# Kernel tuning notes

Hardware: AMD Instinct MI355X
Metric: run time of the kernel (lower is better)

Reference implementation:

```python
import jax, jax.numpy as jnp
import numpy as np

NDIM = 1024
NHEAD = 16
HEAD_DIM = NDIM // NHEAD


def setup_inputs() -> dict:
    key = jax.random.key(0)
    ks = jax.random.split(key, 12)
    B, L, C = 2, 2048, NDIM
    s = 0.02
    return {
        "q": jax.random.normal(ks[0], (B, L, C), jnp.float32),
        "k": jax.random.normal(ks[1], (B, L, C), jnp.float32),
        "v": jax.random.normal(ks[2], (B, L, C), jnp.float32),
        "Wq": jax.random.normal(ks[3], (C, C), jnp.float32) * s,
        "bq": jax.random.normal(ks[4], (C,), jnp.float32) * s,
        "Wk": jax.random.normal(ks[5], (C, C), jnp.float32) * s,
        "bk": jax.random.normal(ks[6], (C,), jnp.float32) * s,
        "Wv": jax.random.normal(ks[7], (C, C), jnp.float32) * s,
        "bv": jax.random.normal(ks[8], (C,), jnp.float32) * s,
        "Wo": jax.random.normal(ks[9], (C, C), jnp.float32) * s,
        "bo": jax.random.normal(ks[10], (C,), jnp.float32) * s,
    }


def reference(q, k, v, Wq, bq, Wk, bk, Wv, bv, Wo, bo):
    B, Lq, C = q.shape
    H, D = NHEAD, HEAD_DIM
    # projections, then split heads: (B, H, L, D)
    qh = (q @ Wq + bq).reshape(B, Lq, H, D).transpose(0, 2, 1, 3)
    kh = (k @ Wk + bk).reshape(B, k.shape[1], H, D).transpose(0, 2, 1, 3)
    vh = (v @ Wv + bv).reshape(B, v.shape[1], H, D).transpose(0, 2, 1, 3)
    scale = 1.0 / jnp.sqrt(jnp.asarray(D, qh.dtype))
    att = jnp.einsum("bhqd,bhkd->bhqk", qh, kh) * scale  # (B,H,Lq,Lk)
    att = jax.nn.softmax(att, axis=-1)  # dropout p=0.0 -> identity
    y = jnp.einsum("bhqk,bhkd->bhqd", att, vh)
    y = y.transpose(0, 2, 1, 3).reshape(B, Lq, C)
    return y @ Wo + bo
```

## Files before the change

### kernel.cpp

```cpp
#include <hip/hip_runtime.h>
#include <math.h>

#define BATCH 2
#define SEQ   2048
#define CDIM  1024
#define NHEAD 16
#define HDIM  64
#define TOKS  (BATCH * SEQ)

typedef __bf16 bf16x8 __attribute__((ext_vector_type(8)));
typedef __bf16 bf16x2 __attribute__((ext_vector_type(2)));
typedef float  f32x4  __attribute__((ext_vector_type(4)));

#define MFMA16(a, b, c) __builtin_amdgcn_mfma_f32_16x16x32_bf16(a, b, c, 0, 0, 0)

#define QSCALE 0.1803368801111204f

__device__ __forceinline__ void gload_lds16(const __bf16* g, __bf16* l) {
    __builtin_amdgcn_global_load_lds(
        (const __attribute__((address_space(1))) unsigned int*)g,
        (__attribute__((address_space(3))) unsigned int*)l, 16, 0, 0);
}

__global__ __launch_bounds__(256) void prep_kernel(
    const float* __restrict__ q, const float* __restrict__ k, const float* __restrict__ v,
    __bf16* __restrict__ qo, __bf16* __restrict__ ko, __bf16* __restrict__ vo,
    const float* __restrict__ W0, const float* __restrict__ W1,
    const float* __restrict__ W2, const float* __restrict__ W3,
    __bf16* __restrict__ T0, __bf16* __restrict__ T1,
    __bf16* __restrict__ T2, __bf16* __restrict__ T3)
{
    __shared__ __bf16 Ts[64][72];
    const int bx = blockIdx.x;
    const int tid = threadIdx.x;

    if (bx < 6144) {
        const int t = bx >> 11;
        const size_t i = ((size_t)(bx & 2047) * 256 + tid) * 8;
        const float* s = t == 0 ? q : (t == 1 ? k : v);
        __bf16* d = t == 0 ? qo : (t == 1 ? ko : vo);
        const float4 x = *(const float4*)&s[i];
        const float4 y = *(const float4*)&s[i + 4];
        bf16x8 o;
        o[0] = (__bf16)x.x; o[1] = (__bf16)x.y; o[2] = (__bf16)x.z; o[3] = (__bf16)x.w;
        o[4] = (__bf16)y.x; o[5] = (__bf16)y.y; o[6] = (__bf16)y.z; o[7] = (__bf16)y.w;
        *(bf16x8*)&d[i] = o;
        return;
    }

    const int t  = bx - 6144;
    const int z  = t >> 8;
    const int ry = (t & 255) >> 4;
    const int rx = t & 15;
    const float* W = z == 0 ? W0 : z == 1 ? W1 : z == 2 ? W2 : W3;
    __bf16* T = z == 0 ? T0 : z == 1 ? T1 : z == 2 ? T2 : T3;
    const int rb = ry * 64, cb = rx * 64;
    const int r = tid >> 4;
    const int c4 = (tid & 15) * 4;
#pragma unroll
    for (int p = 0; p < 4; p++) {
        const int rr = p * 16 + r;
        const float4 w4 = *(const float4*)&W[(size_t)(rb + rr) * CDIM + cb + c4];
        Ts[c4 + 0][rr] = (__bf16)w4.x;
        Ts[c4 + 1][rr] = (__bf16)w4.y;
        Ts[c4 + 2][rr] = (__bf16)w4.z;
        Ts[c4 + 3][rr] = (__bf16)w4.w;
    }
    __syncthreads();
    const int n = tid >> 2;
    const int k16 = (tid & 3) * 16;
    *(bf16x8*)&T[(size_t)(cb + n) * CDIM + rb + k16]     = *(const bf16x8*)&Ts[n][k16];
    *(bf16x8*)&T[(size_t)(cb + n) * CDIM + rb + k16 + 8] = *(const bf16x8*)&Ts[n][k16 + 8];
}

__global__ __launch_bounds__(256) void qkv_gemm_kernel(
    const __bf16* __restrict__ qb, const __bf16* __restrict__ kb,
    const __bf16* __restrict__ vb,
    const __bf16* __restrict__ Wqt, const __bf16* __restrict__ Wkt,
    const __bf16* __restrict__ Wvt,
    const float* __restrict__ bq, const float* __restrict__ bk,
    const float* __restrict__ bv,
    __bf16* __restrict__ Qh, __bf16* __restrict__ Kh, __bf16* __restrict__ Vht)
{
    __shared__ __bf16 As[128 * 32];
    __shared__ __bf16 Bs[128 * 32];

    const int z = blockIdx.z;
    const __bf16* A    = z == 0 ? qb : z == 1 ? kb : Wvt;
    const __bf16* Bt   = z == 0 ? Wqt : z == 1 ? Wkt : vb;
    const float*  bias = z == 0 ? bq : z == 1 ? bk : bv;

    const int tid  = threadIdx.x;
    const int w    = tid >> 6;
    const int lane = tid & 63;
    const int quad = lane >> 4;
    const int c    = lane & 15;
    const int wm   = w >> 1;
    const int wn   = w & 1;
    const int rowBase = (z == 2 ? blockIdx.x : blockIdx.y) * 128;
    const int colBase = (z == 2 ? blockIdx.y : blockIdx.x) * 128;

    const int sr = lane >> 2;
    const int sk = (lane & 3) * 8;

    f32x4 acc[4][4];
#pragma unroll
    for (int i = 0; i < 4; i++)
#pragma unroll
        for (int j = 0; j < 4; j++) acc[i][j] = (f32x4){0, 0, 0, 0};

    for (int k0 = 0; k0 < CDIM; k0 += 32) {
#pragma unroll
        for (int j = 0; j < 2; j++) {
            const int r0 = (w * 2 + j) * 16;
            gload_lds16(A  + (size_t)(rowBase + r0 + sr) * CDIM + k0 + sk, &As[r0 * 32]);
            gload_lds16(Bt + (size_t)(colBase + r0 + sr) * CDIM + k0 + sk, &Bs[r0 * 32]);
        }
        __syncthreads();

        bf16x8 af[4], bf[4];
#pragma unroll
        for (int i = 0; i < 4; i++) {
            af[i] = *(const bf16x8*)&As[(wm * 64 + i * 16 + c) * 32 + quad * 8];
            bf[i] = *(const bf16x8*)&Bs[(wn * 64 + i * 16 + c) * 32 + quad * 8];
        }
#pragma unroll
        for (int mi = 0; mi < 4; mi++)
#pragma unroll
            for (int ni = 0; ni < 4; ni++)
                acc[mi][ni] = MFMA16(af[mi], bf[ni], acc[mi][ni]);
        __syncthreads();
    }

#pragma unroll
    for (int mi = 0; mi < 4; mi++) {
#pragma unroll
        for (int ni = 0; ni < 4; ni++) {
            const int col = colBase + wn * 64 + ni * 16 + c;
#pragma unroll
            for (int r = 0; r < 4; r++) {
                const int row = rowBase + wm * 64 + mi * 16 + quad * 4 + r;
                const float val = acc[mi][ni][r];
                if (z == 2) {
                    const int col2 = (col & ~31) | (((col & 15) << 1) | ((col >> 4) & 1));
                    Vht[(size_t)row * TOKS + col2] = (__bf16)(val + bias[row]);
                } else {
                    const int b = row >> 11, l = row & 2047;
                    const int h = col >> 6,  d = col & 63;
                    const float s = (z == 0) ? QSCALE : 1.0f;
                    __bf16* outp = (z == 0) ? Qh : Kh;
                    outp[((((size_t)b * NHEAD + h) * SEQ) + l) * HDIM + d] =
                        (__bf16)((val + bias[col]) * s);
                }
            }
        }
    }
}

__global__ __launch_bounds__(256) void out_gemm_kernel(
    const __bf16* __restrict__ A, const __bf16* __restrict__ Bt,
    const float* __restrict__ bias, float* __restrict__ out)
{
    __shared__ __bf16 As[128 * 32];
    __shared__ __bf16 Bs[64 * 32];

    const int tid  = threadIdx.x;
    const int w    = tid >> 6;
    const int lane = tid & 63;
    const int quad = lane >> 4;
    const int c    = lane & 15;
    const int wm   = w >> 1;
    const int wn   = w & 1;
    const int rowBase = blockIdx.y * 128;
    const int colBase = blockIdx.x * 64;
    const int sr = lane >> 2;
    const int sk = (lane & 3) * 8;

    f32x4 acc[4][2];
#pragma unroll
    for (int i = 0; i < 4; i++)
#pragma unroll
        for (int j = 0; j < 2; j++) acc[i][j] = (f32x4){0, 0, 0, 0};

    for (int k0 = 0; k0 < CDIM; k0 += 32) {
#pragma unroll
        for (int j = 0; j < 2; j++) {
            const int r0 = (w * 2 + j) * 16;
            gload_lds16(A + (size_t)(rowBase + r0 + sr) * CDIM + k0 + sk, &As[r0 * 32]);
        }
        gload_lds16(Bt + (size_t)(colBase + w * 16 + sr) * CDIM + k0 + sk, &Bs[w * 16 * 32]);
        __syncthreads();

        bf16x8 af[4], bf[2];
#pragma unroll
        for (int i = 0; i < 4; i++)
            af[i] = *(const bf16x8*)&As[(wm * 64 + i * 16 + c) * 32 + quad * 8];
#pragma unroll
        for (int i = 0; i < 2; i++)
            bf[i] = *(const bf16x8*)&Bs[(wn * 32 + i * 16 + c) * 32 + quad * 8];
#pragma unroll
        for (int mi = 0; mi < 4; mi++)
#pragma unroll
            for (int ni = 0; ni < 2; ni++)
                acc[mi][ni] = MFMA16(af[mi], bf[ni], acc[mi][ni]);
        __syncthreads();
    }

#pragma unroll
    for (int mi = 0; mi < 4; mi++) {
#pragma unroll
        for (int ni = 0; ni < 2; ni++) {
            const int col = colBase + wn * 32 + ni * 16 + c;
#pragma unroll
            for (int r = 0; r < 4; r++) {
                const int row = rowBase + wm * 64 + mi * 16 + quad * 4 + r;
                out[(size_t)row * CDIM + col] = acc[mi][ni][r] + bias[col];
            }
        }
    }
}

struct AttnRegs {
    bf16x8 k[4];
    bf16x8 v[4];
};

__global__ __launch_bounds__(64) void attn_v3_kernel(
    const __bf16* __restrict__ Qh, const __bf16* __restrict__ Kh,
    const __bf16* __restrict__ Vht, __bf16* __restrict__ Y)
{
    __shared__ unsigned int Pf[4][16][36];

    const int lane = threadIdx.x;
    const int quad = lane >> 4;
    const int c    = lane & 15;
    const int qt   = blockIdx.x;
    const int bh   = blockIdx.y;
    const int b    = bh >> 4;
    const int h    = bh & 15;
    const int qbase = qt * 64;

    const __bf16* Qg = Qh + (size_t)bh * SEQ * HDIM;
    const __bf16* Kg = Kh + (size_t)bh * SEQ * HDIM;
    const __bf16* Vg = Vht + (size_t)(h * HDIM) * TOKS + (size_t)b * SEQ;

    bf16x8 qf[4][2];
#pragma unroll
    for (int g = 0; g < 4; g++) {
        qf[g][0] = *(const bf16x8*)&Qg[(size_t)(qbase + g * 16 + c) * HDIM + quad * 8];
        qf[g][1] = *(const bf16x8*)&Qg[(size_t)(qbase + g * 16 + c) * HDIM + 32 + quad * 8];
    }

    bf16x8 ones;
#pragma unroll
    for (int j = 0; j < 8; j++) ones[j] = (__bf16)1.0f;

    f32x4 O[4][4];
    f32x4 L[4];
#pragma unroll
    for (int g = 0; g < 4; g++) {
        L[g] = (f32x4){0, 0, 0, 0};
#pragma unroll
        for (int i = 0; i < 4; i++) O[g][i] = (f32x4){0, 0, 0, 0};
    }

    AttnRegs ra, rb;

    const size_t kOff0 = (size_t)c * HDIM + quad * 8;
    const size_t kOff1 = kOff0 + 32;
    const size_t kOff2 = (size_t)(16 + c) * HDIM + quad * 8;
    const size_t kOff3 = kOff2 + 32;

    auto load_tile = [&](AttnRegs& r, int t) {
        r.k[0] = *(const bf16x8*)&Kg[(size_t)t * HDIM + kOff0];
        r.k[1] = *(const bf16x8*)&Kg[(size_t)t * HDIM + kOff1];
        r.k[2] = *(const bf16x8*)&Kg[(size_t)t * HDIM + kOff2];
        r.k[3] = *(const bf16x8*)&Kg[(size_t)t * HDIM + kOff3];
#pragma unroll
        for (int i = 0; i < 4; i++)
            r.v[i] = *(const bf16x8*)&Vg[(size_t)(c + 16 * i) * TOKS + t + quad * 8];
    };

    auto step = [&](const AttnRegs& cur) {
#pragma unroll
        for (int g = 0; g < 4; g++) {
            f32x4 s0 = {0, 0, 0, 0}, s1 = {0, 0, 0, 0};
            s0 = MFMA16(qf[g][0], cur.k[0], s0);
            s0 = MFMA16(qf[g][1], cur.k[1], s0);
            s1 = MFMA16(qf[g][0], cur.k[2], s1);
            s1 = MFMA16(qf[g][1], cur.k[3], s1);
#pragma unroll
            for (int r = 0; r < 4; r++) {
                union { bf16x2 v; unsigned int u; } pk;
                pk.v[0] = (__bf16)__builtin_amdgcn_exp2f(s0[r]);
                pk.v[1] = (__bf16)__builtin_amdgcn_exp2f(s1[r]);
                Pf[g][quad * 4 + r][c] = pk.u;
            }
        }
#pragma unroll
        for (int g = 0; g < 4; g++) {
            const bf16x8 pf = *(const bf16x8*)&Pf[g][c][quad * 4];
            L[g]    = MFMA16(pf, ones, L[g]);
            O[g][0] = MFMA16(pf, cur.v[0], O[g][0]);
            O[g][1] = MFMA16(pf, cur.v[1], O[g][1]);
            O[g][2] = MFMA16(pf, cur.v[2], O[g][2]);
            O[g][3] = MFMA16(pf, cur.v[3], O[g][3]);
        }
    };

    load_tile(ra, 0);
    for (int t0 = 0; t0 < SEQ; t0 += 64) {
        load_tile(rb, (t0 + 32) & (SEQ - 1));
        step(ra);
        load_tile(ra, (t0 + 64) & (SEQ - 1));
        step(rb);
    }

    __bf16* Yb = Y + (size_t)b * SEQ * CDIM;
#pragma unroll
    for (int g = 0; g < 4; g++) {
#pragma unroll
        for (int r = 0; r < 4; r++) {
            const float inv = 1.0f / L[g][r];
            const int l = qbase + g * 16 + quad * 4 + r;
            __bf16* yp = Yb + (size_t)l * CDIM + h * HDIM + c;
            yp[0]  = (__bf16)(O[g][0][r] * inv);
            yp[16] = (__bf16)(O[g][1][r] * inv);
            yp[32] = (__bf16)(O[g][2][r] * inv);
            yp[48] = (__bf16)(O[g][3][r] * inv);
        }
    }
}


extern "C" void kernel_launch(void* const* d_in, const int* in_sizes, int n_in,
                              void* d_out, int out_size, void* d_ws, size_t ws_size,
                              hipStream_t stream)
{
    const float* q  = (const float*)d_in[0];
    const float* k  = (const float*)d_in[1];
    const float* v  = (const float*)d_in[2];
    const float* Wq = (const float*)d_in[3];
    const float* bq = (const float*)d_in[4];
    const float* Wk = (const float*)d_in[5];
    const float* bk = (const float*)d_in[6];
    const float* Wv = (const float*)d_in[7];
    const float* bv = (const float*)d_in[8];
    const float* Wo = (const float*)d_in[9];
    const float* bo = (const float*)d_in[10];
    float* out = (float*)d_out;

    const size_t MAT = (size_t)TOKS * CDIM;
    const size_t WN  = (size_t)CDIM * CDIM;

    __bf16* p   = (__bf16*)d_ws;
    __bf16* qb  = p; p += MAT;
    __bf16* kb  = p; p += MAT;
    __bf16* vb  = p; p += MAT;
    __bf16* Wqt = p; p += WN;
    __bf16* Wkt = p; p += WN;
    __bf16* Wvt = p; p += WN;
    __bf16* Wot = p; p += WN;
    __bf16* Qh  = p; p += MAT;
    __bf16* Kh  = p; p += MAT;
    __bf16* Vht = p; p += MAT;
    __bf16* Yb  = qb;

    prep_kernel<<<dim3(7168), dim3(256), 0, stream>>>(
        q, k, v, qb, kb, vb, Wq, Wk, Wv, Wo, Wqt, Wkt, Wvt, Wot);

    qkv_gemm_kernel<<<dim3(8, 32, 3), dim3(256), 0, stream>>>(
        qb, kb, vb, Wqt, Wkt, Wvt, bq, bk, bv, Qh, Kh, Vht);

    attn_v3_kernel<<<dim3(32, 32), dim3(64), 0, stream>>>(Qh, Kh, Vht, Yb);

    out_gemm_kernel<<<dim3(16, 32), dim3(256), 0, stream>>>(Yb, Wot, bo, out);
}
```

Before: 262.7 us.

## Share K/V tiles across four waves via double-buffered LDS in attention

```diff
diff --git a/kernel.cpp b/kernel.cpp
--- a/kernel.cpp
+++ b/kernel.cpp
@@ -220,25 +220,23 @@
     }
 }
 
-struct AttnRegs {
-    bf16x8 k[4];
-    bf16x8 v[4];
-};
-
-__global__ __launch_bounds__(64) void attn_v3_kernel(
+__global__ __launch_bounds__(256) void attn_v4_kernel(
     const __bf16* __restrict__ Qh, const __bf16* __restrict__ Kh,
     const __bf16* __restrict__ Vht, __bf16* __restrict__ Y)
 {
-    __shared__ unsigned int Pf[4][16][36];
-
-    const int lane = threadIdx.x;
+    __shared__ __align__(16) __bf16 Ks[2][32][72];
+    __shared__ __align__(16) __bf16 Vt[2][64][48];
+    __shared__ __align__(16) unsigned int Pf[4][2][16][36];
+
+    const int tid  = threadIdx.x;
+    const int w    = tid >> 6;
+    const int lane = tid & 63;
     const int quad = lane >> 4;
     const int c    = lane & 15;
-    const int qt   = blockIdx.x;
     const int bh   = blockIdx.y;
     const int b    = bh >> 4;
     const int h    = bh & 15;
-    const int qbase = qt * 64;
+    const int qbase = blockIdx.x * 256 + w * 64;
 
     const __bf16* Qg = Qh + (size_t)bh * SEQ * HDIM;
     const __bf16* Kg = Kh + (size_t)bh * SEQ * HDIM;
@@ -264,56 +262,64 @@
         for (int i = 0; i < 4; i++) O[g][i] = (f32x4){0, 0, 0, 0};
     }
 
-    AttnRegs ra, rb;
-
-    const size_t kOff0 = (size_t)c * HDIM + quad * 8;
-    const size_t kOff1 = kOff0 + 32;
-    const size_t kOff2 = (size_t)(16 + c) * HDIM + quad * 8;
-    const size_t kOff3 = kOff2 + 32;
-
-    auto load_tile = [&](AttnRegs& r, int t) {
-        r.k[0] = *(const bf16x8*)&Kg[(size_t)t * HDIM + kOff0];
-        r.k[1] = *(const bf16x8*)&Kg[(size_t)t * HDIM + kOff1];
-        r.k[2] = *(const bf16x8*)&Kg[(size_t)t * HDIM + kOff2];
-        r.k[3] = *(const bf16x8*)&Kg[(size_t)t * HDIM + kOff3];
-#pragma unroll
-        for (int i = 0; i < 4; i++)
-            r.v[i] = *(const bf16x8*)&Vg[(size_t)(c + 16 * i) * TOKS + t + quad * 8];
-    };
-
-    auto step = [&](const AttnRegs& cur) {
+    const int krow = tid >> 3, kcol = (tid & 7) * 8;
+    const int vrow = tid >> 2, vcol = (tid & 3) * 8;
+
+    {
+        const bf16x8 k0 = *(const bf16x8*)&Kg[(size_t)krow * HDIM + kcol];
+        const bf16x8 v0 = *(const bf16x8*)&Vg[(size_t)vrow * TOKS + vcol];
+        *(bf16x8*)&Ks[0][krow][kcol] = k0;
+        *(bf16x8*)&Vt[0][vrow][vcol] = v0;
+    }
+    __syncthreads();
+
+    int buf = 0;
+    for (int t0 = 0; t0 < SEQ; t0 += 32) {
+        const int tn = t0 + 32;
+        bf16x8 kpre, vpre;
+        if (tn < SEQ) {
+            kpre = *(const bf16x8*)&Kg[(size_t)(tn + krow) * HDIM + kcol];
+            vpre = *(const bf16x8*)&Vg[(size_t)vrow * TOKS + tn + vcol];
+        }
+
+        const bf16x8 k00 = *(const bf16x8*)&Ks[buf][c][quad * 8];
+        const bf16x8 k01 = *(const bf16x8*)&Ks[buf][c][32 + quad * 8];
+        const bf16x8 k10 = *(const bf16x8*)&Ks[buf][16 + c][quad * 8];
+        const bf16x8 k11 = *(const bf16x8*)&Ks[buf][16 + c][32 + quad * 8];
+        const bf16x8 v0 = *(const bf16x8*)&Vt[buf][c][quad * 8];
+        const bf16x8 v1 = *(const bf16x8*)&Vt[buf][16 + c][quad * 8];
+        const bf16x8 v2 = *(const bf16x8*)&Vt[buf][32 + c][quad * 8];
+        const bf16x8 v3 = *(const bf16x8*)&Vt[buf][48 + c][quad * 8];
+
 #pragma unroll
         for (int g = 0; g < 4; g++) {
+            const int pg = g & 1;
             f32x4 s0 = {0, 0, 0, 0}, s1 = {0, 0, 0, 0};
-            s0 = MFMA16(qf[g][0], cur.k[0], s0);
-            s0 = MFMA16(qf[g][1], cur.k[1], s0);
-            s1 = MFMA16(qf[g][0], cur.k[2], s1);
-            s1 = MFMA16(qf[g][1], cur.k[3], s1);
+            s0 = MFMA16(qf[g][0], k00, s0);
+            s0 = MFMA16(qf[g][1], k01, s0);
+            s1 = MFMA16(qf[g][0], k10, s1);
+            s1 = MFMA16(qf[g][1], k11, s1);
 #pragma unroll
             for (int r = 0; r < 4; r++) {
                 union { bf16x2 v; unsigned int u; } pk;
                 pk.v[0] = (__bf16)__builtin_amdgcn_exp2f(s0[r]);
                 pk.v[1] = (__bf16)__builtin_amdgcn_exp2f(s1[r]);
-                Pf[g][quad * 4 + r][c] = pk.u;
+                Pf[w][pg][quad * 4 + r][c] = pk.u;
             }
-        }
-#pragma unroll
-        for (int g = 0; g < 4; g++) {
-            const bf16x8 pf = *(const bf16x8*)&Pf[g][c][quad * 4];
+            const bf16x8 pf = *(const bf16x8*)&Pf[w][pg][c][quad * 4];
             L[g]    = MFMA16(pf, ones, L[g]);
-            O[g][0] = MFMA16(pf, cur.v[0], O[g][0]);
-            O[g][1] = MFMA16(pf, cur.v[1], O[g][1]);
-            O[g][2] = MFMA16(pf, cur.v[2], O[g][2]);
-            O[g][3] = MFMA16(pf, cur.v[3], O[g][3]);
-        }
-    };
-
-    load_tile(ra, 0);
-    for (int t0 = 0; t0 < SEQ; t0 += 64) {
-        load_tile(rb, (t0 + 32) & (SEQ - 1));
-        step(ra);
-        load_tile(ra, (t0 + 64) & (SEQ - 1));
-        step(rb);
+            O[g][0] = MFMA16(pf, v0, O[g][0]);
+            O[g][1] = MFMA16(pf, v1, O[g][1]);
+            O[g][2] = MFMA16(pf, v2, O[g][2]);
+            O[g][3] = MFMA16(pf, v3, O[g][3]);
+        }
+
+        if (tn < SEQ) {
+            *(bf16x8*)&Ks[buf ^ 1][krow][kcol] = kpre;
+            *(bf16x8*)&Vt[buf ^ 1][vrow][vcol] = vpre;
+        }
+        __syncthreads();
+        buf ^= 1;
     }
 
     __bf16* Yb = Y + (size_t)b * SEQ * CDIM;
@@ -372,7 +378,7 @@
     qkv_gemm_kernel<<<dim3(8, 32, 3), dim3(256), 0, stream>>>(
         qb, kb, vb, Wqt, Wkt, Wvt, bq, bk, bv, Qh, Kh, Vht);
 
-    attn_v3_kernel<<<dim3(32, 32), dim3(64), 0, stream>>>(Qh, Kh, Vht, Yb);
+    attn_v4_kernel<<<dim3(SEQ / 256, BATCH * NHEAD), dim3(256), 0, stream>>>(Qh, Kh, Vht, Yb);
 
     out_gemm_kernel<<<dim3(16, 32), dim3(256), 0, stream>>>(Yb, Wot, bo, out);
 }
```

Result: faster. 240.9 us (-8.3%).
